# Optimization experiments

Measured on AMD Instinct MI355X. Metric: run time of the kernel, lower is better.

Reference implementation:

```python
import jax, jax.numpy as jnp
import numpy as np

B, C, H, W = 16, 512, 64, 64
NH = 8  # num_heads


def setup_inputs() -> dict:
    key = jax.random.key(0)
    ks = jax.random.split(key, 7)
    s = 1.0 / np.sqrt(C)
    return {
        "x": jax.random.normal(ks[0], (B, C, H, W), dtype=jnp.float32),
        "wq": jax.random.normal(ks[1], (C, C), dtype=jnp.float32) * s,
        "bq": jax.random.normal(ks[2], (C,), dtype=jnp.float32) * 0.01,
        "wk": jax.random.normal(ks[3], (C, C), dtype=jnp.float32) * s,
        "bk": jax.random.normal(ks[4], (C,), dtype=jnp.float32) * 0.01,
        "wv": jax.random.normal(ks[5], (C, C), dtype=jnp.float32) * s,
        "bv": jax.random.normal(ks[6], (C,), dtype=jnp.float32) * 0.01,
    }


def reference(x, wq, bq, wk, bk, wv, bv):
    b, c_in, h, w = x.shape
    hd = c_in // NH  # head dim

    def conv1x1(wt, bias):
        # 1x1 conv == channel GEMM: (b,c,h,w) x (o,c) -> (b,o,h,w)
        y = jnp.einsum("bchw,oc->bohw", x, wt) + bias[None, :, None, None]
        # view(b, nh, hd, h, w).permute(0,1,3,4,2) -> (b, nh, h, w, hd)
        return y.reshape(b, NH, hd, h, w).transpose(0, 1, 3, 4, 2)

    q = conv1x1(wq, bq)
    k = conv1x1(wk, bk)
    v = conv1x1(wv, bv)

    # attention along the width axis, per (batch, head, row)
    energy = jnp.einsum("bnhqc,bnhkc->bnhqk", q, k)  # (b,nh,h,w,w)
    attn = jax.nn.softmax(energy, axis=-1)
    out = jnp.einsum("bnhqk,bnhkc->bnhqc", attn, v)  # (b,nh,h,w,hd)

    # permute(0,1,4,2,3) -> (b,nh,hd,h,w) -> view(b, C, h, w)
    out = out.transpose(0, 1, 4, 2, 3).reshape(b, c_in, h, w)
    return out + x
```

## Files before the change

### kernel.cpp

```cpp
#include <hip/hip_runtime.h>
#include <stdint.h>

#define B_   16
#define C_   512
#define H_   64
#define W_   64
#define NH_  8
#define HD_  64
#define HW_  4096

typedef __attribute__((ext_vector_type(8))) _Float16 f16x8;
typedef __attribute__((ext_vector_type(8))) unsigned short u16x8;
typedef __attribute__((ext_vector_type(4))) unsigned short u16x4;
typedef __attribute__((ext_vector_type(4))) float f32x4;

static __device__ __forceinline__ unsigned short f2h(float f) {
  _Float16 h = (_Float16)f;
  unsigned short u;
  __builtin_memcpy(&u, &h, 2);
  return u;
}

static __device__ __forceinline__ void gld_lds16(const void* g, void* l) {
  __builtin_amdgcn_global_load_lds((__attribute__((address_space(1))) void*)g,
                                   (__attribute__((address_space(3))) void*)l,
                                   16, 0, 0);
}

__global__ __launch_bounds__(256) void rcca_tr(const float* __restrict__ x,
                                               unsigned short* __restrict__ xT) {
  __shared__ float lT[64 * 65];
  const int bid = blockIdx.x;
  const int st = bid & 63;
  const int ct = (bid >> 6) & 7;
  const int b  = bid >> 9;
  const int t = threadIdx.x;
  const int hwl = t & 63;
  const int cl0 = (t >> 6) * 16;
  const float* src = x + ((size_t)(b * C_ + ct * 64 + cl0)) * HW_ + st * 64 + hwl;
#pragma unroll
  for (int jj = 0; jj < 16; ++jj)
    lT[(cl0 + jj) * 65 + hwl] = src[(size_t)jj * HW_];
  __syncthreads();
  const int hw2 = t >> 2;
  const int cc0 = (t & 3) * 16;
  u16x8 o0, o1;
#pragma unroll
  for (int u = 0; u < 8; ++u) {
    o0[u] = f2h(lT[(cc0 + u) * 65 + hw2]);
    o1[u] = f2h(lT[(cc0 + 8 + u) * 65 + hw2]);
  }
  unsigned short* dst = xT + ((size_t)b * HW_ + st * 64 + hw2) * C_ + ct * 64 + cc0;
  *(u16x8*)dst = o0;
  *(u16x8*)(dst + 8) = o1;
}

__global__ __launch_bounds__(256) void rcca_cvtw(const float* __restrict__ wq,
                                                 const float* __restrict__ wk,
                                                 const float* __restrict__ wv,
                                                 unsigned short* __restrict__ Wc) {
  const int i = blockIdx.x * 256 + threadIdx.x;
  const int e = i * 4;
  const float* w = (e < 262144) ? wq : (e < 524288) ? wk : wv;
  const int off = e & 262143;
  const float4 v = *(const float4*)(w + off);
  u16x4 p;
  p[0] = f2h(v.x); p[1] = f2h(v.y); p[2] = f2h(v.z); p[3] = f2h(v.w);
  *(u16x4*)(Wc + e) = p;
}

__global__ __launch_bounds__(256) void rcca_gemm(const unsigned short* __restrict__ xT,
                                                 const unsigned short* __restrict__ Wc,
                                                 const float* __restrict__ bq,
                                                 const float* __restrict__ bk,
                                                 const float* __restrict__ bv,
                                                 unsigned short* __restrict__ qkv) {
  __shared__ unsigned short lA[128 * 64];
  __shared__ unsigned short lB[128 * 64];
  const int bid = blockIdx.x;
  const int nt = bid % 12;
  const int mt = (bid / 12) & 31;
  const int b  = bid / (12 * 32);
  const int t = threadIdx.x;
  const int wid = t >> 6, lane = t & 63, r = lane & 15, q = lane >> 4;
  const int wm = wid >> 1, wn = wid & 1;
  const unsigned short* Abase = xT + ((size_t)b * HW_ + mt * 128) * C_;
  const unsigned short* Bbase = Wc + (size_t)nt * 128 * C_;
  const int arow = t >> 3;
  const int acol = (t & 7) * 8;
  char* lAb = (char*)lA;
  char* lBb = (char*)lB;
  const int wbase = wid * 1024;
  f32x4 acc[4][4];
#pragma unroll
  for (int i = 0; i < 4; ++i)
#pragma unroll
    for (int j = 0; j < 4; ++j)
      acc[i][j] = (f32x4){0.f, 0.f, 0.f, 0.f};

  for (int k0 = 0; k0 < C_; k0 += 64) {
    __syncthreads();
#pragma unroll
    for (int rr = 0; rr < 4; ++rr) {
      gld_lds16(Abase + (size_t)(rr * 32 + arow) * C_ + k0 + acol, lAb + rr * 4096 + wbase);
      gld_lds16(Bbase + (size_t)(rr * 32 + arow) * C_ + k0 + acol, lBb + rr * 4096 + wbase);
    }
    __syncthreads();
#pragma unroll
    for (int kk = 0; kk < 64; kk += 32) {
      f16x8 av[4], bw[4];
#pragma unroll
      for (int i = 0; i < 4; ++i)
        av[i] = *(const f16x8*)&lA[(wm * 64 + i * 16 + r) * 64 + kk + q * 8];
#pragma unroll
      for (int j = 0; j < 4; ++j)
        bw[j] = *(const f16x8*)&lB[(wn * 64 + j * 16 + r) * 64 + kk + q * 8];
#pragma unroll
      for (int i = 0; i < 4; ++i)
#pragma unroll
        for (int j = 0; j < 4; ++j)
          acc[i][j] = __builtin_amdgcn_mfma_f32_16x16x32_f16(av[i], bw[j], acc[i][j], 0, 0, 0);
    }
  }
  const int headq = nt * 2 + wn;
  const int qsel = headq >> 3;
  const int head = headq & 7;
  const float* bias = (qsel == 0) ? bq : (qsel == 1) ? bk : bv;
  const int h = mt * 2 + wm;
  unsigned short* dst0 = qkv + (size_t)qsel * ((size_t)B_ * NH_ * H_ * W_ * HD_)
                       + (((size_t)b * NH_ + head) * H_ + h) * (size_t)(W_ * HD_);
#pragma unroll
  for (int j = 0; j < 4; ++j) {
    const int d = j * 16 + r;
    const float bias_v = bias[head * 64 + d];
#pragma unroll
    for (int i = 0; i < 4; ++i) {
#pragma unroll
      for (int reg = 0; reg < 4; ++reg) {
        const int w = i * 16 + q * 4 + reg;
        dst0[(size_t)w * HD_ + d] = f2h(acc[i][j][reg] + bias_v);
      }
    }
  }
}

__global__ __launch_bounds__(256) void rcca_attn(const unsigned short* __restrict__ Qb,
                                                 const unsigned short* __restrict__ Kb,
                                                 const unsigned short* __restrict__ Vb,
                                                 const float* __restrict__ x,
                                                 float* __restrict__ out) {
  __shared__ __align__(16) char smem[36864];
  unsigned short* sQ = (unsigned short*)smem;
  unsigned short* sK = (unsigned short*)(smem + 9216);
  unsigned short* sV = (unsigned short*)(smem + 18432);
  unsigned short* sP = (unsigned short*)(smem + 27648);
  float* sO = (float*)smem;
  const int bid = blockIdx.x;
  const int h = bid & 63, head = (bid >> 6) & 7, b = bid >> 9;
  const size_t base = (((size_t)b * NH_ + head) * H_ + h) * (size_t)(W_ * HD_);
  const int t = threadIdx.x;
  {
    const int w = t >> 2, c0 = (t & 3) * 16;
    const size_t off = base + (size_t)t * 16;
    u16x8 a0 = *(const u16x8*)(Qb + off);
    u16x8 a1 = *(const u16x8*)(Qb + off + 8);
    *(u16x8*)&sQ[w * 72 + c0] = a0;
    *(u16x8*)&sQ[w * 72 + c0 + 8] = a1;
    u16x8 k0v = *(const u16x8*)(Kb + off);
    u16x8 k1v = *(const u16x8*)(Kb + off + 8);
    *(u16x8*)&sK[w * 72 + c0] = k0v;
    *(u16x8*)&sK[w * 72 + c0 + 8] = k1v;
    u16x8 v0 = *(const u16x8*)(Vb + off);
    u16x8 v1 = *(const u16x8*)(Vb + off + 8);
#pragma unroll
    for (int jj = 0; jj < 8; ++jj) {
      sV[(c0 + jj) * 72 + w] = v0[jj];
      sV[(c0 + 8 + jj) * 72 + w] = v1[jj];
    }
  }
  __syncthreads();
  const int wv = t >> 6, lane = t & 63, r = lane & 15, q = lane >> 4;
  f32x4 s[4];
#pragma unroll
  for (int j = 0; j < 4; ++j) s[j] = (f32x4){0.f, 0.f, 0.f, 0.f};
#pragma unroll
  for (int kk = 0; kk < 64; kk += 32) {
    f16x8 aq = *(const f16x8*)&sQ[(wv * 16 + r) * 72 + kk + q * 8];
#pragma unroll
    for (int j = 0; j < 4; ++j) {
      f16x8 bk8 = *(const f16x8*)&sK[(j * 16 + r) * 72 + kk + q * 8];
      s[j] = __builtin_amdgcn_mfma_f32_16x16x32_f16(aq, bk8, s[j], 0, 0, 0);
    }
  }
  float inv[4];
#pragma unroll
  for (int reg = 0; reg < 4; ++reg) {
    float mx = fmaxf(fmaxf(s[0][reg], s[1][reg]), fmaxf(s[2][reg], s[3][reg]));
#pragma unroll
    for (int o = 1; o < 16; o <<= 1) mx = fmaxf(mx, __shfl_xor(mx, o, 64));
    float p0 = __expf(s[0][reg] - mx);
    float p1 = __expf(s[1][reg] - mx);
    float p2 = __expf(s[2][reg] - mx);
    float p3 = __expf(s[3][reg] - mx);
    float sum = p0 + p1 + p2 + p3;
#pragma unroll
    for (int o = 1; o < 16; o <<= 1) sum += __shfl_xor(sum, o, 64);
    inv[reg] = 1.0f / sum;
    const int row = wv * 16 + q * 4 + reg;
    sP[row * 72 + 0 + r]  = f2h(p0);
    sP[row * 72 + 16 + r] = f2h(p1);
    sP[row * 72 + 32 + r] = f2h(p2);
    sP[row * 72 + 48 + r] = f2h(p3);
  }
  __syncthreads();
  f32x4 o4[4];
#pragma unroll
  for (int j = 0; j < 4; ++j) o4[j] = (f32x4){0.f, 0.f, 0.f, 0.f};
#pragma unroll
  for (int kk = 0; kk < 64; kk += 32) {
    f16x8 ap = *(const f16x8*)&sP[(wv * 16 + r) * 72 + kk + q * 8];
#pragma unroll
    for (int jd = 0; jd < 4; ++jd) {
      f16x8 bv8 = *(const f16x8*)&sV[(jd * 16 + r) * 72 + kk + q * 8];
      o4[jd] = __builtin_amdgcn_mfma_f32_16x16x32_f16(ap, bv8, o4[jd], 0, 0, 0);
    }
  }
#pragma unroll
  for (int jd = 0; jd < 4; ++jd) {
    const int d = jd * 16 + r;
#pragma unroll
    for (int reg = 0; reg < 4; ++reg) {
      const int w = wv * 16 + q * 4 + reg;
      sO[d * 66 + w] = o4[jd][reg] * inv[reg];
    }
  }
  __syncthreads();
  const int d = t >> 2, w0 = (t & 3) * 16;
  const size_t obase = ((size_t)b * C_ + head * 64 + d) * HW_ + h * 64 + w0;
  const float4* xr = (const float4*)(x + obase);
  float4* op = (float4*)(out + obase);
#pragma unroll
  for (int u = 0; u < 4; ++u) {
    float4 xv = xr[u];
    float4 ov;
    ov.x = sO[d * 66 + w0 + u * 4 + 0] + xv.x;
    ov.y = sO[d * 66 + w0 + u * 4 + 1] + xv.y;
    ov.z = sO[d * 66 + w0 + u * 4 + 2] + xv.z;
    ov.w = sO[d * 66 + w0 + u * 4 + 3] + xv.w;
    op[u] = ov;
  }
}

extern "C" void kernel_launch(void* const* d_in, const int* in_sizes, int n_in,
                              void* d_out, int out_size, void* d_ws, size_t ws_size,
                              hipStream_t stream) {
  const float* x  = (const float*)d_in[0];
  const float* wq = (const float*)d_in[1];
  const float* bq = (const float*)d_in[2];
  const float* wk = (const float*)d_in[3];
  const float* bk = (const float*)d_in[4];
  const float* wv = (const float*)d_in[5];
  const float* bv = (const float*)d_in[6];
  float* out = (float*)d_out;
  char* ws = (char*)d_ws;
  unsigned short* xT = (unsigned short*)ws;
  unsigned short* Wc = (unsigned short*)(ws + (size_t)67108864);
  unsigned short* Qb = (unsigned short*)(ws + (size_t)68681728);
  unsigned short* Kb = Qb + (size_t)33554432;
  unsigned short* Vb = Kb + (size_t)33554432;
  hipLaunchKernelGGL(rcca_tr,   dim3(8192), dim3(256), 0, stream, x, xT);
  hipLaunchKernelGGL(rcca_cvtw, dim3(768),  dim3(256), 0, stream, wq, wk, wv, Wc);
  hipLaunchKernelGGL(rcca_gemm, dim3(6144), dim3(256), 0, stream, xT, Wc, bq, bk, bv, Qb);
  hipLaunchKernelGGL(rcca_attn, dim3(8192), dim3(256), 0, stream, Qb, Kb, Vb, x, out);
}
```

Baseline: 476.4 us.

## Swizzle GEMM LDS tiles, stage epilogue through LDS, reorder V transpose loads

Adds an XOR swizzle to the GEMM's LDS tile layout, applied both to the global-to-LDS load column and to the MFMA operand reads, to cut bank conflicts. The GEMM epilogue now writes biased fp16 results into a padded LDS tile and then emits 16-byte vector stores per output row. Previously each lane wrote scattered 2-byte global stores. In the attention kernel, the V load mapping is changed so that consecutive threads write consecutive columns of the transposed sV tile, reducing LDS bank conflicts. The cost is extra shared memory and two added barriers in the GEMM.

```diff
diff --git a/kernel.cpp b/kernel.cpp
--- a/kernel.cpp
+++ b/kernel.cpp
@@ -75,19 +75,22 @@
                                                  const float* __restrict__ bk,
                                                  const float* __restrict__ bv,
                                                  unsigned short* __restrict__ qkv) {
-  __shared__ unsigned short lA[128 * 64];
-  __shared__ unsigned short lB[128 * 64];
+  __shared__ __align__(16) char gsm[34816];
+  unsigned short* lA = (unsigned short*)gsm;
+  unsigned short* lB = (unsigned short*)(gsm + 16384);
+  unsigned short* sT = (unsigned short*)gsm;
   const int bid = blockIdx.x;
   const int nt = bid % 12;
   const int mt = (bid / 12) & 31;
   const int b  = bid / (12 * 32);
   const int t = threadIdx.x;
   const int wid = t >> 6, lane = t & 63, r = lane & 15, q = lane >> 4;
+  const int rx = r & 7;
   const int wm = wid >> 1, wn = wid & 1;
   const unsigned short* Abase = xT + ((size_t)b * HW_ + mt * 128) * C_;
   const unsigned short* Bbase = Wc + (size_t)nt * 128 * C_;
   const int arow = t >> 3;
-  const int acol = (t & 7) * 8;
+  const int acol = (((t & 7) ^ ((t >> 3) & 7)) * 8);
   char* lAb = (char*)lA;
   char* lBb = (char*)lB;
   const int wbase = wid * 1024;
@@ -108,13 +111,14 @@
     __syncthreads();
 #pragma unroll
     for (int kk = 0; kk < 64; kk += 32) {
+      const int cbase = kk >> 3;
       f16x8 av[4], bw[4];
 #pragma unroll
       for (int i = 0; i < 4; ++i)
-        av[i] = *(const f16x8*)&lA[(wm * 64 + i * 16 + r) * 64 + kk + q * 8];
+        av[i] = *(const f16x8*)&lA[(wm * 64 + i * 16 + r) * 64 + (((cbase + q) ^ rx) * 8)];
 #pragma unroll
       for (int j = 0; j < 4; ++j)
-        bw[j] = *(const f16x8*)&lB[(wn * 64 + j * 16 + r) * 64 + kk + q * 8];
+        bw[j] = *(const f16x8*)&lB[(wn * 64 + j * 16 + r) * 64 + (((cbase + q) ^ rx) * 8)];
 #pragma unroll
       for (int i = 0; i < 4; ++i)
 #pragma unroll
@@ -122,26 +126,37 @@
           acc[i][j] = __builtin_amdgcn_mfma_f32_16x16x32_f16(av[i], bw[j], acc[i][j], 0, 0, 0);
     }
   }
+  __syncthreads();
   const int headq = nt * 2 + wn;
   const int qsel = headq >> 3;
   const int head = headq & 7;
   const float* bias = (qsel == 0) ? bq : (qsel == 1) ? bk : bv;
-  const int h = mt * 2 + wm;
-  unsigned short* dst0 = qkv + (size_t)qsel * ((size_t)B_ * NH_ * H_ * W_ * HD_)
-                       + (((size_t)b * NH_ + head) * H_ + h) * (size_t)(W_ * HD_);
 #pragma unroll
   for (int j = 0; j < 4; ++j) {
-    const int d = j * 16 + r;
-    const float bias_v = bias[head * 64 + d];
+    const float bias_v = bias[head * 64 + j * 16 + r];
 #pragma unroll
     for (int i = 0; i < 4; ++i) {
 #pragma unroll
       for (int reg = 0; reg < 4; ++reg) {
-        const int w = i * 16 + q * 4 + reg;
-        dst0[(size_t)w * HD_ + d] = f2h(acc[i][j][reg] + bias_v);
+        const int m = wm * 64 + i * 16 + q * 4 + reg;
+        const int n = wn * 64 + j * 16 + r;
+        sT[m * 136 + n] = f2h(acc[i][j][reg] + bias_v);
       }
     }
   }
+  __syncthreads();
+  const int wr = t >> 1, half = t & 1;
+  const int hq2 = nt * 2 + half;
+  const int qs2 = hq2 >> 3;
+  const int hd2 = hq2 & 7;
+  const int h2 = mt * 2 + (wr >> 6);
+  const int w2 = wr & 63;
+  unsigned short* dstb = qkv + (size_t)qs2 * ((size_t)B_ * NH_ * H_ * W_ * HD_)
+                       + (((size_t)b * NH_ + hd2) * H_ + h2) * (size_t)(W_ * HD_)
+                       + (size_t)w2 * HD_;
+#pragma unroll
+  for (int u = 0; u < 8; ++u)
+    *(u16x8*)(dstb + u * 8) = *(const u16x8*)&sT[wr * 136 + half * 64 + u * 8];
 }
 
 __global__ __launch_bounds__(256) void rcca_attn(const unsigned short* __restrict__ Qb,
@@ -170,12 +185,14 @@
     u16x8 k1v = *(const u16x8*)(Kb + off + 8);
     *(u16x8*)&sK[w * 72 + c0] = k0v;
     *(u16x8*)&sK[w * 72 + c0 + 8] = k1v;
-    u16x8 v0 = *(const u16x8*)(Vb + off);
-    u16x8 v1 = *(const u16x8*)(Vb + off + 8);
+    const int wv2 = t & 63, cv0 = (t >> 6) * 16;
+    const size_t voff = base + (size_t)wv2 * HD_ + cv0;
+    u16x8 v0 = *(const u16x8*)(Vb + voff);
+    u16x8 v1 = *(const u16x8*)(Vb + voff + 8);
 #pragma unroll
     for (int jj = 0; jj < 8; ++jj) {
-      sV[(c0 + jj) * 72 + w] = v0[jj];
-      sV[(c0 + 8 + jj) * 72 + w] = v1[jj];
+      sV[(cv0 + jj) * 72 + wv2] = v0[jj];
+      sV[(cv0 + 8 + jj) * 72 + wv2] = v1[jj];
     }
   }
   __syncthreads();
```

Result: no change. 474.3 us (-0.4%).

## Fuse QKV projection GEMM with row attention in one kernel

Applied to the files above, without the earlier changes.

Replaces the separate QKV GEMM and attention kernels with one kernel per (batch, row). It computes Q, K and V for two heads at a time straight into shared memory, then runs softmax attention on them. This removes the global write and re-read of the large fp16 Q/K/V intermediates. In exchange, the GEMM operands come from global/L2 without LDS staging, two of the eight waves sit idle during the GEMM, and the output stores are strided and poorly coalesced. The residual is now read from the fp16 transposed copy of x rather than the fp32 input, which costs some precision.

```diff
diff --git a/kernel.cpp b/kernel.cpp
--- a/kernel.cpp
+++ b/kernel.cpp
@@ -20,11 +20,10 @@
   __builtin_memcpy(&u, &h, 2);
   return u;
 }
-
-static __device__ __forceinline__ void gld_lds16(const void* g, void* l) {
-  __builtin_amdgcn_global_load_lds((__attribute__((address_space(1))) void*)g,
-                                   (__attribute__((address_space(3))) void*)l,
-                                   16, 0, 0);
+static __device__ __forceinline__ float h2f(unsigned short u) {
+  _Float16 h;
+  __builtin_memcpy(&h, &u, 2);
+  return (float)h;
 }
 
 __global__ __launch_bounds__(256) void rcca_tr(const float* __restrict__ x,
@@ -69,185 +68,153 @@
   *(u16x4*)(Wc + e) = p;
 }
 
-__global__ __launch_bounds__(256) void rcca_gemm(const unsigned short* __restrict__ xT,
-                                                 const unsigned short* __restrict__ Wc,
-                                                 const float* __restrict__ bq,
-                                                 const float* __restrict__ bk,
-                                                 const float* __restrict__ bv,
-                                                 unsigned short* __restrict__ qkv) {
-  __shared__ unsigned short lA[128 * 64];
-  __shared__ unsigned short lB[128 * 64];
+__global__ __launch_bounds__(512, 4) void rcca_fused(const unsigned short* __restrict__ xT,
+                                                     const unsigned short* __restrict__ Wc,
+                                                     const float* __restrict__ bq,
+                                                     const float* __restrict__ bk,
+                                                     const float* __restrict__ bv,
+                                                     float* __restrict__ out) {
+  __shared__ __align__(16) unsigned short smem[6 * 64 * 72];
+  unsigned short* buf[2][3];
+  buf[0][0] = smem;
+  buf[0][1] = smem + 4608;
+  buf[0][2] = smem + 9216;
+  buf[1][0] = smem + 13824;
+  buf[1][1] = smem + 18432;
+  buf[1][2] = smem + 23040;
+
   const int bid = blockIdx.x;
-  const int nt = bid % 12;
-  const int mt = (bid / 12) & 31;
-  const int b  = bid / (12 * 32);
+  const int b = bid >> 6, h = bid & 63;
   const int t = threadIdx.x;
   const int wid = t >> 6, lane = t & 63, r = lane & 15, q = lane >> 4;
-  const int wm = wid >> 1, wn = wid & 1;
-  const unsigned short* Abase = xT + ((size_t)b * HW_ + mt * 128) * C_;
-  const unsigned short* Bbase = Wc + (size_t)nt * 128 * C_;
-  const int arow = t >> 3;
-  const int acol = (t & 7) * 8;
-  char* lAb = (char*)lA;
-  char* lBb = (char*)lB;
-  const int wbase = wid * 1024;
-  f32x4 acc[4][4];
-#pragma unroll
-  for (int i = 0; i < 4; ++i)
-#pragma unroll
-    for (int j = 0; j < 4; ++j)
-      acc[i][j] = (f32x4){0.f, 0.f, 0.f, 0.f};
-
-  for (int k0 = 0; k0 < C_; k0 += 64) {
-    __syncthreads();
-#pragma unroll
-    for (int rr = 0; rr < 4; ++rr) {
-      gld_lds16(Abase + (size_t)(rr * 32 + arow) * C_ + k0 + acol, lAb + rr * 4096 + wbase);
-      gld_lds16(Bbase + (size_t)(rr * 32 + arow) * C_ + k0 + acol, lBb + rr * 4096 + wbase);
+  const unsigned short* Aslice = xT + ((size_t)b * HW_ + h * 64) * C_;
+
+  const int mat = wid >> 1;
+  const int half = wid & 1;
+  const float* biasm = (mat == 0) ? bq : (mat == 1) ? bk : bv;
+
+  for (int hp = 0; hp < 4; ++hp) {
+    if (wid < 6) {
+      f32x4 acc[4][4];
+#pragma unroll
+      for (int i = 0; i < 4; ++i)
+#pragma unroll
+        for (int j = 0; j < 4; ++j)
+          acc[i][j] = (f32x4){0.f, 0.f, 0.f, 0.f};
+      const unsigned short* Brow[4];
+#pragma unroll
+      for (int j = 0; j < 4; ++j) {
+        const int head = hp * 2 + (j >> 1);
+        const int n = mat * 512 + head * 64 + half * 32 + (j & 1) * 16 + r;
+        Brow[j] = Wc + (size_t)n * C_;
+      }
+      const unsigned short* Arow[4];
+#pragma unroll
+      for (int i = 0; i < 4; ++i)
+        Arow[i] = Aslice + (size_t)(i * 16 + r) * C_;
+#pragma unroll 4
+      for (int kk = 0; kk < 16; ++kk) {
+        const int k = kk * 32 + q * 8;
+        f16x8 av[4], bw[4];
+#pragma unroll
+        for (int i = 0; i < 4; ++i) av[i] = *(const f16x8*)(Arow[i] + k);
+#pragma unroll
+        for (int j = 0; j < 4; ++j) bw[j] = *(const f16x8*)(Brow[j] + k);
+#pragma unroll
+        for (int i = 0; i < 4; ++i)
+#pragma unroll
+          for (int j = 0; j < 4; ++j)
+            acc[i][j] = __builtin_amdgcn_mfma_f32_16x16x32_f16(av[i], bw[j], acc[i][j], 0, 0, 0);
+      }
+#pragma unroll
+      for (int j = 0; j < 4; ++j) {
+        const int hl = j >> 1;
+        const int d = half * 32 + (j & 1) * 16 + r;
+        const int head = hp * 2 + hl;
+        const float bias_v = biasm[head * 64 + d];
+        if (mat < 2) {
+          unsigned short* dst = buf[hl][mat];
+#pragma unroll
+          for (int i = 0; i < 4; ++i)
+#pragma unroll
+            for (int reg = 0; reg < 4; ++reg)
+              dst[(i * 16 + q * 4 + reg) * 72 + d] = f2h(acc[i][j][reg] + bias_v);
+        } else {
+          unsigned short* dst = buf[hl][2];
+#pragma unroll
+          for (int i = 0; i < 4; ++i)
+#pragma unroll
+            for (int reg = 0; reg < 4; ++reg)
+              dst[d * 72 + (i * 16 + q * 4 + reg)] = f2h(acc[i][j][reg] + bias_v);
+        }
+      }
     }
     __syncthreads();
-#pragma unroll
-    for (int kk = 0; kk < 64; kk += 32) {
-      f16x8 av[4], bw[4];
-#pragma unroll
-      for (int i = 0; i < 4; ++i)
-        av[i] = *(const f16x8*)&lA[(wm * 64 + i * 16 + r) * 64 + kk + q * 8];
-#pragma unroll
-      for (int j = 0; j < 4; ++j)
-        bw[j] = *(const f16x8*)&lB[(wn * 64 + j * 16 + r) * 64 + kk + q * 8];
-#pragma unroll
-      for (int i = 0; i < 4; ++i)
-#pragma unroll
-        for (int j = 0; j < 4; ++j)
-          acc[i][j] = __builtin_amdgcn_mfma_f32_16x16x32_f16(av[i], bw[j], acc[i][j], 0, 0, 0);
+    {
+      const int hl = wid >> 2;
+      const int wv = wid & 3;
+      const int head = hp * 2 + hl;
+      unsigned short* sQ = buf[hl][0];
+      unsigned short* sK = buf[hl][1];
+      unsigned short* sVT = buf[hl][2];
+      unsigned short* sP = sQ;
+      f32x4 s[4];
+#pragma unroll
+      for (int j = 0; j < 4; ++j) s[j] = (f32x4){0.f, 0.f, 0.f, 0.f};
+#pragma unroll
+      for (int kk = 0; kk < 64; kk += 32) {
+        f16x8 aq = *(const f16x8*)&sQ[(wv * 16 + r) * 72 + kk + q * 8];
+#pragma unroll
+        for (int j = 0; j < 4; ++j) {
+          f16x8 bk8 = *(const f16x8*)&sK[(j * 16 + r) * 72 + kk + q * 8];
+          s[j] = __builtin_amdgcn_mfma_f32_16x16x32_f16(aq, bk8, s[j], 0, 0, 0);
+        }
+      }
+      float inv[4];
+#pragma unroll
+      for (int reg = 0; reg < 4; ++reg) {
+        float mx = fmaxf(fmaxf(s[0][reg], s[1][reg]), fmaxf(s[2][reg], s[3][reg]));
+#pragma unroll
+        for (int o = 1; o < 16; o <<= 1) mx = fmaxf(mx, __shfl_xor(mx, o, 64));
+        float p0 = __expf(s[0][reg] - mx);
+        float p1 = __expf(s[1][reg] - mx);
+        float p2 = __expf(s[2][reg] - mx);
+        float p3 = __expf(s[3][reg] - mx);
+        float sum = p0 + p1 + p2 + p3;
+#pragma unroll
+        for (int o = 1; o < 16; o <<= 1) sum += __shfl_xor(sum, o, 64);
+        inv[reg] = 1.0f / sum;
+        const int row = wv * 16 + q * 4 + reg;
+        sP[row * 72 + 0 + r]  = f2h(p0);
+        sP[row * 72 + 16 + r] = f2h(p1);
+        sP[row * 72 + 32 + r] = f2h(p2);
+        sP[row * 72 + 48 + r] = f2h(p3);
+      }
+      f32x4 o4[4];
+#pragma unroll
+      for (int j = 0; j < 4; ++j) o4[j] = (f32x4){0.f, 0.f, 0.f, 0.f};
+#pragma unroll
+      for (int kk = 0; kk < 64; kk += 32) {
+        f16x8 ap = *(const f16x8*)&sP[(wv * 16 + r) * 72 + kk + q * 8];
+#pragma unroll
+        for (int jd = 0; jd < 4; ++jd) {
+          f16x8 bv8 = *(const f16x8*)&sVT[(jd * 16 + r) * 72 + kk + q * 8];
+          o4[jd] = __builtin_amdgcn_mfma_f32_16x16x32_f16(ap, bv8, o4[jd], 0, 0, 0);
+        }
+      }
+#pragma unroll
+      for (int jd = 0; jd < 4; ++jd) {
+        const int d = jd * 16 + r;
+        const int c = head * 64 + d;
+#pragma unroll
+        for (int reg = 0; reg < 4; ++reg) {
+          const int w = wv * 16 + q * 4 + reg;
+          const float res = h2f(Aslice[(size_t)w * C_ + c]);
+          out[((size_t)(b * C_ + c) * H_ + h) * W_ + w] = o4[jd][reg] * inv[reg] + res;
+        }
+      }
     }
-  }
-  const int headq = nt * 2 + wn;
-  const int qsel = headq >> 3;
-  const int head = headq & 7;
-  const float* bias = (qsel == 0) ? bq : (qsel == 1) ? bk : bv;
-  const int h = mt * 2 + wm;
-  unsigned short* dst0 = qkv + (size_t)qsel * ((size_t)B_ * NH_ * H_ * W_ * HD_)
-                       + (((size_t)b * NH_ + head) * H_ + h) * (size_t)(W_ * HD_);
-#pragma unroll
-  for (int j = 0; j < 4; ++j) {
-    const int d = j * 16 + r;
-    const float bias_v = bias[head * 64 + d];
-#pragma unroll
-    for (int i = 0; i < 4; ++i) {
-#pragma unroll
-      for (int reg = 0; reg < 4; ++reg) {
-        const int w = i * 16 + q * 4 + reg;
-        dst0[(size_t)w * HD_ + d] = f2h(acc[i][j][reg] + bias_v);
-      }
-    }
-  }
-}
-
-__global__ __launch_bounds__(256) void rcca_attn(const unsigned short* __restrict__ Qb,
-                                                 const unsigned short* __restrict__ Kb,
-                                                 const unsigned short* __restrict__ Vb,
-                                                 const float* __restrict__ x,
-                                                 float* __restrict__ out) {
-  __shared__ __align__(16) char smem[36864];
-  unsigned short* sQ = (unsigned short*)smem;
-  unsigned short* sK = (unsigned short*)(smem + 9216);
-  unsigned short* sV = (unsigned short*)(smem + 18432);
-  unsigned short* sP = (unsigned short*)(smem + 27648);
-  float* sO = (float*)smem;
-  const int bid = blockIdx.x;
-  const int h = bid & 63, head = (bid >> 6) & 7, b = bid >> 9;
-  const size_t base = (((size_t)b * NH_ + head) * H_ + h) * (size_t)(W_ * HD_);
-  const int t = threadIdx.x;
-  {
-    const int w = t >> 2, c0 = (t & 3) * 16;
-    const size_t off = base + (size_t)t * 16;
-    u16x8 a0 = *(const u16x8*)(Qb + off);
-    u16x8 a1 = *(const u16x8*)(Qb + off + 8);
-    *(u16x8*)&sQ[w * 72 + c0] = a0;
-    *(u16x8*)&sQ[w * 72 + c0 + 8] = a1;
-    u16x8 k0v = *(const u16x8*)(Kb + off);
-    u16x8 k1v = *(const u16x8*)(Kb + off + 8);
-    *(u16x8*)&sK[w * 72 + c0] = k0v;
-    *(u16x8*)&sK[w * 72 + c0 + 8] = k1v;
-    u16x8 v0 = *(const u16x8*)(Vb + off);
-    u16x8 v1 = *(const u16x8*)(Vb + off + 8);
-#pragma unroll
-    for (int jj = 0; jj < 8; ++jj) {
-      sV[(c0 + jj) * 72 + w] = v0[jj];
-      sV[(c0 + 8 + jj) * 72 + w] = v1[jj];
-    }
-  }
-  __syncthreads();
-  const int wv = t >> 6, lane = t & 63, r = lane & 15, q = lane >> 4;
-  f32x4 s[4];
-#pragma unroll
-  for (int j = 0; j < 4; ++j) s[j] = (f32x4){0.f, 0.f, 0.f, 0.f};
-#pragma unroll
-  for (int kk = 0; kk < 64; kk += 32) {
-    f16x8 aq = *(const f16x8*)&sQ[(wv * 16 + r) * 72 + kk + q * 8];
-#pragma unroll
-    for (int j = 0; j < 4; ++j) {
-      f16x8 bk8 = *(const f16x8*)&sK[(j * 16 + r) * 72 + kk + q * 8];
-      s[j] = __builtin_amdgcn_mfma_f32_16x16x32_f16(aq, bk8, s[j], 0, 0, 0);
-    }
-  }
-  float inv[4];
-#pragma unroll
-  for (int reg = 0; reg < 4; ++reg) {
-    float mx = fmaxf(fmaxf(s[0][reg], s[1][reg]), fmaxf(s[2][reg], s[3][reg]));
-#pragma unroll
-    for (int o = 1; o < 16; o <<= 1) mx = fmaxf(mx, __shfl_xor(mx, o, 64));
-    float p0 = __expf(s[0][reg] - mx);
-    float p1 = __expf(s[1][reg] - mx);
-    float p2 = __expf(s[2][reg] - mx);
-    float p3 = __expf(s[3][reg] - mx);
-    float sum = p0 + p1 + p2 + p3;
-#pragma unroll
-    for (int o = 1; o < 16; o <<= 1) sum += __shfl_xor(sum, o, 64);
-    inv[reg] = 1.0f / sum;
-    const int row = wv * 16 + q * 4 + reg;
-    sP[row * 72 + 0 + r]  = f2h(p0);
-    sP[row * 72 + 16 + r] = f2h(p1);
-    sP[row * 72 + 32 + r] = f2h(p2);
-    sP[row * 72 + 48 + r] = f2h(p3);
-  }
-  __syncthreads();
-  f32x4 o4[4];
-#pragma unroll
-  for (int j = 0; j < 4; ++j) o4[j] = (f32x4){0.f, 0.f, 0.f, 0.f};
-#pragma unroll
-  for (int kk = 0; kk < 64; kk += 32) {
-    f16x8 ap = *(const f16x8*)&sP[(wv * 16 + r) * 72 + kk + q * 8];
-#pragma unroll
-    for (int jd = 0; jd < 4; ++jd) {
-      f16x8 bv8 = *(const f16x8*)&sV[(jd * 16 + r) * 72 + kk + q * 8];
-      o4[jd] = __builtin_amdgcn_mfma_f32_16x16x32_f16(ap, bv8, o4[jd], 0, 0, 0);
-    }
-  }
-#pragma unroll
-  for (int jd = 0; jd < 4; ++jd) {
-    const int d = jd * 16 + r;
-#pragma unroll
-    for (int reg = 0; reg < 4; ++reg) {
-      const int w = wv * 16 + q * 4 + reg;
-      sO[d * 66 + w] = o4[jd][reg] * inv[reg];
-    }
-  }
-  __syncthreads();
-  const int d = t >> 2, w0 = (t & 3) * 16;
-  const size_t obase = ((size_t)b * C_ + head * 64 + d) * HW_ + h * 64 + w0;
-  const float4* xr = (const float4*)(x + obase);
-  float4* op = (float4*)(out + obase);
-#pragma unroll
-  for (int u = 0; u < 4; ++u) {
-    float4 xv = xr[u];
-    float4 ov;
-    ov.x = sO[d * 66 + w0 + u * 4 + 0] + xv.x;
-    ov.y = sO[d * 66 + w0 + u * 4 + 1] + xv.y;
-    ov.z = sO[d * 66 + w0 + u * 4 + 2] + xv.z;
-    ov.w = sO[d * 66 + w0 + u * 4 + 3] + xv.w;
-    op[u] = ov;
+    __syncthreads();
   }
 }
 
@@ -265,11 +232,7 @@
   char* ws = (char*)d_ws;
   unsigned short* xT = (unsigned short*)ws;
   unsigned short* Wc = (unsigned short*)(ws + (size_t)67108864);
-  unsigned short* Qb = (unsigned short*)(ws + (size_t)68681728);
-  unsigned short* Kb = Qb + (size_t)33554432;
-  unsigned short* Vb = Kb + (size_t)33554432;
-  hipLaunchKernelGGL(rcca_tr,   dim3(8192), dim3(256), 0, stream, x, xT);
-  hipLaunchKernelGGL(rcca_cvtw, dim3(768),  dim3(256), 0, stream, wq, wk, wv, Wc);
-  hipLaunchKernelGGL(rcca_gemm, dim3(6144), dim3(256), 0, stream, xT, Wc, bq, bk, bv, Qb);
-  hipLaunchKernelGGL(rcca_attn, dim3(8192), dim3(256), 0, stream, Qb, Kb, Vb, x, out);
-}
+  hipLaunchKernelGGL(rcca_tr,    dim3(8192), dim3(256), 0, stream, x, xT);
+  hipLaunchKernelGGL(rcca_cvtw,  dim3(768),  dim3(256), 0, stream, wq, wk, wv, Wc);
+  hipLaunchKernelGGL(rcca_fused, dim3(1024), dim3(512), 0, stream, xT, Wc, bq, bk, bv, out);
+}
```

Result: slower. 789.5 us (+65.7%).
